# Performance work log

Hardware: AMD Instinct MI355X
Metric: run time of the kernel (lower is better)

The kernel has to match this reference:

```python
import jax, jax.numpy as jnp
import numpy as np

B, N, D = 64, 8192, 128
REPLACE = 0.0  # stands in for torch.inf default; kept finite for numerics


def setup_inputs() -> dict:
    key = jax.random.key(0)
    k1, k2 = jax.random.split(key)
    X = jax.random.normal(k1, (B, N, D), dtype=jnp.float32)
    # mask True == position masked OUT (module computes ~mask to get valid)
    mask = jax.random.randint(k2, (B, N), 0, 2) == 1
    W = jnp.ones((D,), dtype=jnp.float32)
    b = jnp.zeros((D,), dtype=jnp.float32)
    return {"X": X, "mask": mask, "W": W, "b": b}


def reference(X, mask, W, b):
    # valid positions: ~mask, broadcast across feature dim
    valid = (~mask)[:, :, None].astype(X.dtype)          # [B, N, 1]
    count = jnp.sum(valid, axis=1)                       # [B, 1]
    mean = jnp.sum(X * valid, axis=1) / count            # [B, D]
    centered = X - mean[:, None, :]                      # [B, N, D]
    # torch masked std is unbiased (ddof=1)
    var = jnp.sum((centered * centered) * valid, axis=1) / (count - 1.0)
    std = jnp.sqrt(var)                                  # [B, D]
    normed = centered / std[:, None, :]                  # [B, N, D]
    # diag_embed(W) + F.linear == elementwise affine
    out = normed * W + b
    # masked positions were filled with REPLACE before the affine step
    out = jnp.where(mask[:, :, None], REPLACE * W + b, out)
    return out
```

## Files before the change

kernel.cpp:

```cpp
#include <hip/hip_runtime.h>

#define B_ 64
#define N_ 8192
#define D_ 128
#define D4 (D_ / 4)
#define NCHUNKS 32
#define CHUNK (N_ / NCHUNKS)

typedef float v4f __attribute__((ext_vector_type(4)));

#define WS_SUMP  0
#define WS_SQP   (B_ * NCHUNKS * D_)
#define WS_CNTP  (2 * B_ * NCHUNKS * D_)
#define WS_SCALE (2 * B_ * NCHUNKS * D_ + B_ * NCHUNKS)
#define WS_SHIFT (WS_SCALE + B_ * D_)

__global__ __launch_bounds__(256) void reduce_kernel(
        const float* __restrict__ X, const int* __restrict__ mask,
        float* __restrict__ ws) {
    const int b   = blockIdx.x;
    const int cy  = blockIdx.y;
    const int tid = threadIdx.x;
    const int q   = tid & 31;
    const int sub = tid >> 5;
    const int n0  = cy * CHUNK;

    __shared__ float valid[CHUNK];
    valid[tid] = (mask[b * N_ + n0 + tid] == 0) ? 1.0f : 0.0f;
    __syncthreads();

    const v4f* __restrict__ Xr =
        (const v4f*)(X + (size_t)b * N_ * D_) + (size_t)n0 * D4 + q;

    v4f s  = (v4f)(0.f);
    v4f ss = (v4f)(0.f);
    float cnt = 0.f;

    #pragma unroll
    for (int k = 0; k < CHUNK / 8; ++k) {
        const int n = sub + 8 * k;
        const float v = valid[n];
        cnt += v;
        if (v != 0.0f) {
            const v4f x = Xr[(size_t)n * D4];
            s += x;
            ss += x * x;
        }
    }

    __shared__ v4f sh_s[8][32];
    __shared__ v4f sh_ss[8][32];
    __shared__ float sh_c[8];
    sh_s[sub][q]  = s;
    sh_ss[sub][q] = ss;
    if (q == 0) sh_c[sub] = cnt;
    __syncthreads();

    if (sub == 0) {
        v4f ts = s, tss = ss;
        #pragma unroll
        for (int k = 1; k < 8; ++k) {
            ts  += sh_s[k][q];
            tss += sh_ss[k][q];
        }
        v4f* __restrict__ sump = (v4f*)(ws + WS_SUMP);
        v4f* __restrict__ sqp  = (v4f*)(ws + WS_SQP);
        const int slot = (b * NCHUNKS + cy) * D4 + q;
        sump[slot] = ts;
        sqp[slot]  = tss;
    }
    if (tid == 0) {
        float c = 0.f;
        #pragma unroll
        for (int k = 0; k < 8; ++k) c += sh_c[k];
        ws[WS_CNTP + b * NCHUNKS + cy] = c;
    }
}

__global__ __launch_bounds__(256) void finalize_kernel(
        const float* __restrict__ W, const float* __restrict__ bias,
        float* __restrict__ ws) {
    const float* __restrict__ sump = ws + WS_SUMP;
    const float* __restrict__ sqp  = ws + WS_SQP;
    const float* __restrict__ cntp = ws + WS_CNTP;
    float* __restrict__ scale = ws + WS_SCALE;
    float* __restrict__ shift = ws + WS_SHIFT;

    const int i = blockIdx.x * blockDim.x + threadIdx.x;
    if (i >= B_ * D_) return;
    const int b = i >> 7;
    const int d = i & (D_ - 1);

    float c = 0.f, s = 0.f, sq = 0.f;
    #pragma unroll
    for (int cy = 0; cy < NCHUNKS; ++cy) {
        c  += cntp[b * NCHUNKS + cy];
        s  += sump[(b * NCHUNKS + cy) * D_ + d];
        sq += sqp [(b * NCHUNKS + cy) * D_ + d];
    }
    const float mean = s / c;
    const float var  = (sq - s * mean) / (c - 1.0f);
    const float sc   = W[d] * rsqrtf(var);
    scale[i] = sc;
    shift[i] = bias[d] - mean * sc;
}

__global__ __launch_bounds__(256) void normalize_kernel(
        const float* __restrict__ X, const int* __restrict__ mask,
        const float* __restrict__ ws, const float* __restrict__ bias,
        float* __restrict__ out) {
    const v4f* __restrict__ X4 = (const v4f*)X;
    v4f* __restrict__ O4 = (v4f*)out;
    const v4f* __restrict__ S4 = (const v4f*)(ws + WS_SCALE);
    const v4f* __restrict__ H4 = (const v4f*)(ws + WS_SHIFT);
    const v4f* __restrict__ B4 = (const v4f*)bias;

    const int i   = blockIdx.x * 256 + threadIdx.x;
    const int row = i >> 5;
    const int c   = i & 31;
    const int b   = row >> 13;

    if (mask[row] != 0) {
        __builtin_nontemporal_store(B4[c], &O4[i]);
    } else {
        const v4f x  = X4[i];
        const v4f sc = S4[(b << 5) + c];
        const v4f sh = H4[(b << 5) + c];
        __builtin_nontemporal_store(x * sc + sh, &O4[i]);
    }
}

extern "C" void kernel_launch(void* const* d_in, const int* in_sizes, int n_in,
                              void* d_out, int out_size, void* d_ws, size_t ws_size,
                              hipStream_t stream) {
    const float* X    = (const float*)d_in[0];
    const int*   mask = (const int*)d_in[1];
    const float* W    = (const float*)d_in[2];
    const float* bias = (const float*)d_in[3];
    float* out = (float*)d_out;
    float* ws  = (float*)d_ws;

    reduce_kernel<<<dim3(B_, NCHUNKS), 256, 0, stream>>>(X, mask, ws);

    finalize_kernel<<<(B_ * D_ + 255) / 256, 256, 0, stream>>>(W, bias, ws);

    normalize_kernel<<<(B_ * N_ * D4) / 256, 256, 0, stream>>>(X, mask, ws, bias, out);
}
```

Baseline: 436.0 us.

## Fuse reduce, finalize and normalize into one cooperative kernel with grid sync

Replaces the three-kernel pipeline with one cooperative kernel. Each block compacts its valid and masked row indices with ballot and popcount, reduces sums over the valid rows, and synchronizes the whole grid. It then computes scale and shift per block and writes the output from the same chunk. The aim is to remove two launches, the scale/shift round trip through memory and the per-row mask branching, and to reuse X from cache for the second pass. In exchange it depends on co-residency of 1024 blocks, pays for a grid-wide barrier, and falls back to the old path if the cooperative launch is not possible.

Result: no change. 435.6 us (-0.1%).

```diff
diff --git a/kernel.cpp b/kernel.cpp
--- a/kernel.cpp
+++ b/kernel.cpp
@@ -1,14 +1,130 @@
 #include <hip/hip_runtime.h>
+#include <hip/hip_cooperative_groups.h>
+
+namespace cg = cooperative_groups;
 
 #define B_ 64
 #define N_ 8192
 #define D_ 128
 #define D4 (D_ / 4)
+
+typedef float v4f __attribute__((ext_vector_type(4)));
+
+#define NCH 16
+#define CHROWS (N_ / NCH)
+
+#define FW_SUM 0
+#define FW_SQ  (B_ * NCH * D_)
+#define FW_CNT (2 * B_ * NCH * D_)
+
+__global__ __launch_bounds__(256, 4) void fused_kernel(
+        const float* __restrict__ X, const int* __restrict__ mask,
+        const float* __restrict__ W, const float* __restrict__ bias,
+        float* __restrict__ out, float* __restrict__ ws) {
+    const int b   = blockIdx.x;
+    const int cy  = blockIdx.y;
+    const int tid = threadIdx.x;
+    const int q   = tid & 31;
+    const int sub = tid >> 5;
+    const int n0  = cy * CHROWS;
+
+    __shared__ unsigned long long wmask[8];
+    __shared__ unsigned short rows[CHROWS];
+    __shared__ unsigned short mrows[CHROWS];
+    __shared__ v4f sh_s[8][32];
+    __shared__ v4f sh_ss[8][32];
+    __shared__ v4f sc4[D4], sh4[D4], b4[D4];
+
+    const int lane = tid & 63;
+    const int wv   = tid >> 6;
+    const int m0 = mask[b * N_ + n0 + tid];
+    const int m1 = mask[b * N_ + n0 + 256 + tid];
+    const unsigned long long bal0 = __ballot(m0 == 0);
+    const unsigned long long bal1 = __ballot(m1 == 0);
+    if (lane == 0) { wmask[wv] = bal0; wmask[wv + 4] = bal1; }
+    __syncthreads();
+    int pre[8];
+    int acc = 0;
+    #pragma unroll
+    for (int g = 0; g < 8; ++g) { pre[g] = acc; acc += __popcll(wmask[g]); }
+    const int nvalid = acc;
+    {
+        const unsigned long long below = (1ull << lane) - 1ull;
+        const int rv0 = pre[wv] + __popcll(bal0 & below);
+        if (m0 == 0) rows[rv0] = (unsigned short)tid;
+        else         mrows[tid - rv0] = (unsigned short)tid;
+        const int j1 = tid + 256;
+        const int rv1 = pre[wv + 4] + __popcll(bal1 & below);
+        if (m1 == 0) rows[rv1] = (unsigned short)j1;
+        else         mrows[j1 - rv1] = (unsigned short)j1;
+    }
+    __syncthreads();
+
+    const v4f* __restrict__ Xr = (const v4f*)(X + ((size_t)b * N_ + n0) * D_) + q;
+    v4f*       __restrict__ Or = (v4f*)(out + ((size_t)b * N_ + n0) * D_) + q;
+
+    v4f s = (v4f)(0.f), ss = (v4f)(0.f);
+    const int nmain = nvalid & ~7;
+    #pragma unroll 4
+    for (int j = sub; j < nmain; j += 8) {
+        const int row = rows[j];
+        const v4f x = Xr[(size_t)row * D4];
+        s += x; ss += x * x;
+    }
+    if (nmain + sub < nvalid) {
+        const int row = rows[nmain + sub];
+        const v4f x = Xr[(size_t)row * D4];
+        s += x; ss += x * x;
+    }
+
+    sh_s[sub][q] = s; sh_ss[sub][q] = ss;
+    __syncthreads();
+    if (sub == 0) {
+        v4f ts = s, tss = ss;
+        #pragma unroll
+        for (int k = 1; k < 8; ++k) { ts += sh_s[k][q]; tss += sh_ss[k][q]; }
+        ((v4f*)(ws + FW_SUM))[(b * NCH + cy) * D4 + q] = ts;
+        ((v4f*)(ws + FW_SQ ))[(b * NCH + cy) * D4 + q] = tss;
+    }
+    if (tid == 0) ws[FW_CNT + b * NCH + cy] = (float)nvalid;
+
+    cg::this_grid().sync();
+
+    if (tid < D_) {
+        const int d = tid;
+        float c = 0.f, su = 0.f, sq = 0.f;
+        #pragma unroll
+        for (int k = 0; k < NCH; ++k) {
+            c  += ws[FW_CNT + b * NCH + k];
+            su += ws[FW_SUM + (b * NCH + k) * D_ + d];
+            sq += ws[FW_SQ  + (b * NCH + k) * D_ + d];
+        }
+        const float mean = su / c;
+        const float var  = (sq - su * mean) / (c - 1.0f);
+        const float scv  = W[d] * rsqrtf(var);
+        ((float*)sc4)[d] = scv;
+        ((float*)sh4)[d] = bias[d] - mean * scv;
+    }
+    if (tid < D4) b4[tid] = ((const v4f*)bias)[tid];
+    __syncthreads();
+
+    const v4f scq = sc4[q], shq = sh4[q], bq = b4[q];
+    #pragma unroll 4
+    for (int j = sub; j < nvalid; j += 8) {
+        const int row = rows[j];
+        const v4f x = Xr[(size_t)row * D4];
+        __builtin_nontemporal_store(x * scq + shq, &Or[(size_t)row * D4]);
+    }
+    const int nmask = CHROWS - nvalid;
+    #pragma unroll 4
+    for (int j = sub; j < nmask; j += 8) {
+        const int row = mrows[j];
+        __builtin_nontemporal_store(bq, &Or[(size_t)row * D4]);
+    }
+}
+
 #define NCHUNKS 32
 #define CHUNK (N_ / NCHUNKS)
-
-typedef float v4f __attribute__((ext_vector_type(4)));
-
 #define WS_SUMP  0
 #define WS_SQP   (B_ * NCHUNKS * D_)
 #define WS_CNTP  (2 * B_ * NCHUNKS * D_)
@@ -35,7 +151,6 @@
     v4f s  = (v4f)(0.f);
     v4f ss = (v4f)(0.f);
     float cnt = 0.f;
-
     #pragma unroll
     for (int k = 0; k < CHUNK / 8; ++k) {
         const int n = sub + 8 * k;
@@ -63,11 +178,8 @@
             ts  += sh_s[k][q];
             tss += sh_ss[k][q];
         }
-        v4f* __restrict__ sump = (v4f*)(ws + WS_SUMP);
-        v4f* __restrict__ sqp  = (v4f*)(ws + WS_SQP);
-        const int slot = (b * NCHUNKS + cy) * D4 + q;
-        sump[slot] = ts;
-        sqp[slot]  = tss;
+        ((v4f*)(ws + WS_SUMP))[(b * NCHUNKS + cy) * D4 + q] = ts;
+        ((v4f*)(ws + WS_SQP ))[(b * NCHUNKS + cy) * D4 + q] = tss;
     }
     if (tid == 0) {
         float c = 0.f;
@@ -80,12 +192,6 @@
 __global__ __launch_bounds__(256) void finalize_kernel(
         const float* __restrict__ W, const float* __restrict__ bias,
         float* __restrict__ ws) {
-    const float* __restrict__ sump = ws + WS_SUMP;
-    const float* __restrict__ sqp  = ws + WS_SQP;
-    const float* __restrict__ cntp = ws + WS_CNTP;
-    float* __restrict__ scale = ws + WS_SCALE;
-    float* __restrict__ shift = ws + WS_SHIFT;
-
     const int i = blockIdx.x * blockDim.x + threadIdx.x;
     if (i >= B_ * D_) return;
     const int b = i >> 7;
@@ -94,15 +200,15 @@
     float c = 0.f, s = 0.f, sq = 0.f;
     #pragma unroll
     for (int cy = 0; cy < NCHUNKS; ++cy) {
-        c  += cntp[b * NCHUNKS + cy];
-        s  += sump[(b * NCHUNKS + cy) * D_ + d];
-        sq += sqp [(b * NCHUNKS + cy) * D_ + d];
+        c  += ws[WS_CNTP + b * NCHUNKS + cy];
+        s  += ws[WS_SUMP + (b * NCHUNKS + cy) * D_ + d];
+        sq += ws[WS_SQP  + (b * NCHUNKS + cy) * D_ + d];
     }
     const float mean = s / c;
     const float var  = (sq - s * mean) / (c - 1.0f);
     const float sc   = W[d] * rsqrtf(var);
-    scale[i] = sc;
-    shift[i] = bias[d] - mean * sc;
+    ws[WS_SCALE + i] = sc;
+    ws[WS_SHIFT + i] = bias[d] - mean * sc;
 }
 
 __global__ __launch_bounds__(256) void normalize_kernel(
@@ -140,9 +246,30 @@
     float* out = (float*)d_out;
     float* ws  = (float*)d_ws;
 
+    static int coop_ok = -1;
+    if (coop_ok < 0) {
+        int maxb = 0;
+        hipError_t e1 = hipOccupancyMaxActiveBlocksPerMultiprocessor(
+            &maxb, fused_kernel, 256, 0);
+        int nCU = 256;
+        hipDeviceProp_t prop;
+        int dev = 0;
+        if (hipGetDevice(&dev) == hipSuccess &&
+            hipGetDeviceProperties(&prop, dev) == hipSuccess)
+            nCU = prop.multiProcessorCount;
+        coop_ok = (e1 == hipSuccess && maxb * nCU >= B_ * NCH) ? 1 : 0;
+    }
+
+    if (coop_ok == 1) {
+        void* args[] = {(void*)&X, (void*)&mask, (void*)&W, (void*)&bias,
+                        (void*)&out, (void*)&ws};
+        hipError_t e = hipLaunchCooperativeKernel(
+            (const void*)fused_kernel, dim3(B_, NCH), dim3(256), args, 0, stream);
+        if (e == hipSuccess) return;
+        coop_ok = 0;
+    }
+
     reduce_kernel<<<dim3(B_, NCHUNKS), 256, 0, stream>>>(X, mask, ws);
-
     finalize_kernel<<<(B_ * D_ + 255) / 256, 256, 0, stream>>>(W, bias, ws);
-
     normalize_kernel<<<(B_ * N_ * D4) / 256, 256, 0, stream>>>(X, mask, ws, bias, out);
 }
```
